# Optimization experiments

Hardware: AMD Instinct MI355X
Metric: run time of the kernel (lower is better)

Reference implementation:

```python
import jax, jax.numpy as jnp
import numpy as np

B, P, Q, O, H = 2048, 32, 65, 16, 32

def setup_inputs() -> dict:
    key = jax.random.key(0)
    ks = jax.random.split(key, 13)
    s1 = 1.0           # fan_in = 1 for Linear(1,H)
    sH = 1.0 / np.sqrt(H)
    return {
        "x": jax.random.normal(ks[0], (B, P), dtype=jnp.float32),
        # psi_{p,q}: 1 -> H -> H -> 1 MLPs, stacked over (P, Q)
        "psi_w1": jax.random.normal(ks[1], (P, Q, H), dtype=jnp.float32) * s1,
        "psi_b1": jax.random.normal(ks[2], (P, Q, H), dtype=jnp.float32) * s1,
        "psi_w2": jax.random.normal(ks[3], (P, Q, H, H), dtype=jnp.float32) * sH,
        "psi_b2": jax.random.normal(ks[4], (P, Q, H), dtype=jnp.float32) * sH,
        "psi_w3": jax.random.normal(ks[5], (P, Q, H), dtype=jnp.float32) * sH,
        "psi_b3": jax.random.normal(ks[6], (P, Q), dtype=jnp.float32) * sH,
        # phi_{q,i}: 1 -> H -> H -> 1 MLPs, stacked over (Q, O)
        "phi_w1": jax.random.normal(ks[7], (Q, O, H), dtype=jnp.float32) * s1,
        "phi_b1": jax.random.normal(ks[8], (Q, O, H), dtype=jnp.float32) * s1,
        "phi_w2": jax.random.normal(ks[9], (Q, O, H, H), dtype=jnp.float32) * sH,
        "phi_b2": jax.random.normal(ks[10], (Q, O, H), dtype=jnp.float32) * sH,
        "phi_w3": jax.random.normal(ks[11], (Q, O, H), dtype=jnp.float32) * sH,
        "phi_b3": jax.random.normal(ks[12], (Q, O), dtype=jnp.float32) * sH,
    }

def reference(x, psi_w1, psi_b1, psi_w2, psi_b2, psi_w3, psi_b3,
              phi_w1, phi_b1, phi_w2, phi_b2, phi_w3, phi_b3):
    # Inner functions psi_{p,q}(x_p): all P*Q tiny MLPs batched together.
    h = jnp.tanh(x[:, :, None, None] * psi_w1 + psi_b1)                 # [B,P,Q,H]
    h = jnp.tanh(jnp.einsum('bpqh,pqhk->bpqk', h, psi_w2) + psi_b2)     # [B,P,Q,H]
    psi = jnp.einsum('bpqh,pqh->bpq', h, psi_w3) + psi_b3               # [B,P,Q]
    s = psi.sum(axis=1)                                                 # [B,Q]  (sum over p)
    # Outer functions phi_{q,i}(s_q): all Q*O tiny MLPs batched together.
    g = jnp.tanh(s[:, :, None, None] * phi_w1 + phi_b1)                 # [B,Q,O,H]
    g = jnp.tanh(jnp.einsum('bqoh,qohk->bqok', g, phi_w2) + phi_b2)     # [B,Q,O,H]
    phi = jnp.einsum('bqoh,qoh->bqo', g, phi_w3) + phi_b3               # [B,Q,O]
    return phi.sum(axis=1)                                              # [B,O]  (sum over q)
```

## Files before the change

kernel.cpp:

```cpp
#include <hip/hip_runtime.h>
#include <hip/hip_bf16.h>

#define B_ 2048
#define P_ 32
#define Q_ 65
#define O_ 16
#define H_ 32

typedef __attribute__((ext_vector_type(8))) short short8;
typedef __attribute__((ext_vector_type(4))) float f32x4;

union F4S8 { float4 f; short8 s; unsigned u[4]; };

#if defined(__has_builtin)
# if __has_builtin(__builtin_amdgcn_exp2f)
#  define HAVE_EXP2 1
# endif
#endif
#ifdef HAVE_EXP2
#define SCALE_K 2.8853900817779268f
__device__ __forceinline__ float exp_z(float y) { return __builtin_amdgcn_exp2f(y); }
#else
#define SCALE_K 2.0f
__device__ __forceinline__ float exp_z(float y) { return __expf(y); }
#endif

__device__ __forceinline__ float sigc(float y) {
    return __builtin_amdgcn_rcpf(exp_z(y) + 1.0f);
}

__device__ __forceinline__ unsigned short bf_rne(float f) {
    unsigned u = __float_as_uint(f);
    return (unsigned short)((u + 0x7FFFu + ((u >> 16) & 1u)) >> 16);
}

__device__ __forceinline__ unsigned pk_bf16(float a, float b) {
    __hip_bfloat162 h = __float22bfloat162_rn(make_float2(a, b));
    return *reinterpret_cast<unsigned*>(&h);
}

struct Rec {
    float4 w1a, w1b, b1a, b1b;
    float4 h0, l0, h1, l1;
    float4 ms;
};

template<int MODE>
__device__ __forceinline__ Rec load_rec(
    const float* __restrict__ fragc, const float* __restrict__ shw,
    const float* __restrict__ w1, const float* __restrict__ b1,
    const float* __restrict__ w2, const float* __restrict__ b2,
    const float* __restrict__ w3,
    int pq, int lane, int g, int col)
{
    Rec r;
    if (MODE == 2) {
        const float4* fp = reinterpret_cast<const float4*>(fragc) + (size_t)pq * 256 + lane;
        r.h0 = fp[0]; r.l0 = fp[64]; r.h1 = fp[128]; r.l1 = fp[192];
        const float4* a = reinterpret_cast<const float4*>(shw + (size_t)pq * 128);
        r.w1a = a[g * 2];     r.w1b = a[g * 2 + 1];
        r.b1a = a[8 + g * 2]; r.b1b = a[8 + g * 2 + 1];
        r.ms  = a[16 + col];
    } else {
        const float4* w1p = reinterpret_cast<const float4*>(w1 + pq * H_ + g * 8);
        r.w1a = w1p[0]; r.w1b = w1p[1];
        const float4* b1p = reinterpret_cast<const float4*>(b1 + pq * H_ + g * 8);
        r.b1a = b1p[0]; r.b1b = b1p[1];
        const float* w2p = w2 + (size_t)pq * (H_ * H_);
        F4S8 u0, u1, u2, u3;
        float cs0 = 0.f, cs1 = 0.f;
        #pragma unroll
        for (int jj = 0; jj < 8; ++jj) {
            float v0 = -2.f * SCALE_K * w2p[(g * 8 + jj) * H_ + col];
            float v1 = -2.f * SCALE_K * w2p[(g * 8 + jj) * H_ + 16 + col];
            unsigned q0 = __float_as_uint(v0);
            u0.s[jj] = (short)(q0 >> 16);
            u1.s[jj] = (short)(__float_as_uint(v0 - __uint_as_float(q0 & 0xFFFF0000u)) >> 16);
            unsigned q1 = __float_as_uint(v1);
            u2.s[jj] = (short)(q1 >> 16);
            u3.s[jj] = (short)(__float_as_uint(v1 - __uint_as_float(q1 & 0xFFFF0000u)) >> 16);
        }
        for (int h = 0; h < H_; ++h) {
            cs0 += w2p[h * H_ + col];
            cs1 += w2p[h * H_ + 16 + col];
        }
        r.h0 = u0.f; r.l0 = u1.f; r.h1 = u2.f; r.l1 = u3.f;
        r.ms = make_float4(SCALE_K * (b2[pq * H_ + col] + cs0),
                           SCALE_K * (b2[pq * H_ + 16 + col] + cs1),
                           -2.f * w3[pq * H_ + col],
                           -2.f * w3[pq * H_ + 16 + col]);
    }
    return r;
}

template<bool PRE>
__device__ __forceinline__ void eval_rec(const Rec& r, float xv, float psum[4])
{
    float s0 = sigc(PRE ? fmaf(xv, r.w1a.x, r.b1a.x) : SCALE_K * fmaf(xv, r.w1a.x, r.b1a.x));
    float s1 = sigc(PRE ? fmaf(xv, r.w1a.y, r.b1a.y) : SCALE_K * fmaf(xv, r.w1a.y, r.b1a.y));
    float s2 = sigc(PRE ? fmaf(xv, r.w1a.z, r.b1a.z) : SCALE_K * fmaf(xv, r.w1a.z, r.b1a.z));
    float s3 = sigc(PRE ? fmaf(xv, r.w1a.w, r.b1a.w) : SCALE_K * fmaf(xv, r.w1a.w, r.b1a.w));
    float s4 = sigc(PRE ? fmaf(xv, r.w1b.x, r.b1b.x) : SCALE_K * fmaf(xv, r.w1b.x, r.b1b.x));
    float s5 = sigc(PRE ? fmaf(xv, r.w1b.y, r.b1b.y) : SCALE_K * fmaf(xv, r.w1b.y, r.b1b.y));
    float s6 = sigc(PRE ? fmaf(xv, r.w1b.z, r.b1b.z) : SCALE_K * fmaf(xv, r.w1b.z, r.b1b.z));
    float s7 = sigc(PRE ? fmaf(xv, r.w1b.w, r.b1b.w) : SCALE_K * fmaf(xv, r.w1b.w, r.b1b.w));

    F4S8 hi, lo;
    hi.u[0] = pk_bf16(s0, s1); hi.u[1] = pk_bf16(s2, s3);
    hi.u[2] = pk_bf16(s4, s5); hi.u[3] = pk_bf16(s6, s7);
    float l0v = s0 - __uint_as_float(hi.u[0] << 16);
    float l1v = s1 - __uint_as_float(hi.u[0] & 0xFFFF0000u);
    float l2v = s2 - __uint_as_float(hi.u[1] << 16);
    float l3v = s3 - __uint_as_float(hi.u[1] & 0xFFFF0000u);
    float l4v = s4 - __uint_as_float(hi.u[2] << 16);
    float l5v = s5 - __uint_as_float(hi.u[2] & 0xFFFF0000u);
    float l6v = s6 - __uint_as_float(hi.u[3] << 16);
    float l7v = s7 - __uint_as_float(hi.u[3] & 0xFFFF0000u);
    lo.u[0] = pk_bf16(l0v, l1v); lo.u[1] = pk_bf16(l2v, l3v);
    lo.u[2] = pk_bf16(l4v, l5v); lo.u[3] = pk_bf16(l6v, l7v);

    F4S8 c0, c1, c2, c3;
    c0.f = r.h0; c1.f = r.l0; c2.f = r.h1; c3.f = r.l1;
    f32x4 acc0 = {r.ms.x, r.ms.x, r.ms.x, r.ms.x};
    f32x4 acc1 = {r.ms.y, r.ms.y, r.ms.y, r.ms.y};
    acc0 = __builtin_amdgcn_mfma_f32_16x16x32_bf16(hi.s, c0.s, acc0, 0, 0, 0);
    acc0 = __builtin_amdgcn_mfma_f32_16x16x32_bf16(lo.s, c0.s, acc0, 0, 0, 0);
    acc0 = __builtin_amdgcn_mfma_f32_16x16x32_bf16(hi.s, c1.s, acc0, 0, 0, 0);
    acc1 = __builtin_amdgcn_mfma_f32_16x16x32_bf16(hi.s, c2.s, acc1, 0, 0, 0);
    acc1 = __builtin_amdgcn_mfma_f32_16x16x32_bf16(lo.s, c2.s, acc1, 0, 0, 0);
    acc1 = __builtin_amdgcn_mfma_f32_16x16x32_bf16(hi.s, c3.s, acc1, 0, 0, 0);

    #pragma unroll
    for (int rr = 0; rr < 4; ++rr) {
        psum[rr] = fmaf(sigc(acc0[rr]), r.ms.z, psum[rr]);
        psum[rr] = fmaf(sigc(acc1[rr]), r.ms.w, psum[rr]);
    }
}

__device__ __forceinline__ void reduce_store(float psum[4], float b3sum,
                                             int lane, int g, int b0w,
                                             float* addr_base, int stride, bool atomic)
{
    #pragma unroll
    for (int rr = 0; rr < 4; ++rr) {
        psum[rr] += __shfl_xor(psum[rr], 1);
        psum[rr] += __shfl_xor(psum[rr], 2);
        psum[rr] += __shfl_xor(psum[rr], 4);
        psum[rr] += __shfl_xor(psum[rr], 8);
    }
    float v01 = (lane & 1) ? psum[1] : psum[0];
    float v23 = (lane & 1) ? psum[3] : psum[2];
    float v = (lane & 2) ? v23 : v01;
    if ((lane & 15) < 4) {
        int row = b0w + g * 4 + (lane & 3);
        float* a = addr_base + (size_t)row * stride;
        if (atomic) atomicAdd(a, v + b3sum);
        else        *a = v + b3sum;
    }
}

template<int MODE>
__global__ __launch_bounds__(256)
void psi_main(const float* __restrict__ x, const float* __restrict__ xT,
              const float* __restrict__ w1, const float* __restrict__ b1,
              const float* __restrict__ w2, const float* __restrict__ b2,
              const float* __restrict__ w3, const float* __restrict__ b3,
              const float* __restrict__ b3c,
              const float* __restrict__ fragc, const float* __restrict__ shw,
              float* __restrict__ sT)
{
    const int id = blockIdx.x;
    const int j = (id & 7) * 260 + (id >> 3);
    const int q = j >> 5;
    const int btile = j & 31;
    const int lane = threadIdx.x & 63;
    const int wid = threadIdx.x >> 6;
    const int g = lane >> 4, col = lane & 15;
    const int b0w = btile * 64 + wid * 16;

    float psum[4] = {0.f, 0.f, 0.f, 0.f};
    float b3sum = (MODE == 2) ? b3c[q] : 0.f;

    Rec cur = load_rec<MODE>(fragc, shw, w1, b1, w2, b2, w3, q, lane, g, col);
    float xv = (MODE == 2) ? xT[b0w + col] : x[(size_t)(b0w + col) * P_];

    #pragma unroll 2
    for (int p = 0; p < P_; ++p) {
        const int pn = (p + 1 < P_) ? p + 1 : P_ - 1;
        Rec nxt = load_rec<MODE>(fragc, shw, w1, b1, w2, b2, w3,
                                 pn * Q_ + q, lane, g, col);
        float xn = (MODE == 2) ? xT[(size_t)pn * B_ + b0w + col]
                               : x[(size_t)(b0w + col) * P_ + pn];
        if (MODE != 2) {
            float ws = 0.f;
            for (int h = 0; h < H_; ++h) ws += w3[(p * Q_ + q) * H_ + h];
            b3sum += b3[p * Q_ + q] + ws;
        }
        eval_rec<(MODE == 2)>(cur, xv, psum);
        cur = nxt; xv = xn;
    }

    reduce_store(psum, b3sum, lane, g, b0w, sT + (size_t)q * B_, 1, false);
}

template<int MODE>
__global__ __launch_bounds__(256)
void phi_main(const float* __restrict__ sT,
              const float* __restrict__ w1, const float* __restrict__ b1,
              const float* __restrict__ w2, const float* __restrict__ b2,
              const float* __restrict__ w3, const float* __restrict__ b3,
              const float* __restrict__ b3g,
              const float* __restrict__ fragc, const float* __restrict__ shw,
              float* __restrict__ out)
{
    const int id = blockIdx.x;
    const int j = (id & 7) * 256 + (id >> 3);
    const int qg = j >> 9;
    const int rem = j & 511;
    const int o = rem >> 5;
    const int btile = rem & 31;
    const int lane = threadIdx.x & 63;
    const int wid = threadIdx.x >> 6;
    const int g = lane >> 4, col = lane & 15;
    const int b0w = btile * 64 + wid * 16;

    const int q0  = (qg == 0) ? 0 : 17 + (qg - 1) * 16;
    const int len = (qg == 0) ? 17 : 16;

    float psum[4] = {0.f, 0.f, 0.f, 0.f};
    float b3sum = (MODE == 2) ? b3g[qg * O_ + o] : 0.f;

    Rec cur = load_rec<MODE>(fragc, shw, w1, b1, w2, b2, w3, q0 * O_ + o, lane, g, col);
    float sv = sT[(size_t)q0 * B_ + b0w + col];

    #pragma unroll 2
    for (int i = 0; i < len; ++i) {
        const int in_ = (i + 1 < len) ? i + 1 : len - 1;
        const int qn = q0 + in_;
        Rec nxt = load_rec<MODE>(fragc, shw, w1, b1, w2, b2, w3,
                                 qn * O_ + o, lane, g, col);
        float sn = sT[(size_t)qn * B_ + b0w + col];
        if (MODE != 2) {
            float ws = 0.f;
            for (int h = 0; h < H_; ++h) ws += w3[((q0 + i) * O_ + o) * H_ + h];
            b3sum += b3[(q0 + i) * O_ + o] + ws;
        }
        eval_rec<(MODE == 2)>(cur, sv, psum);
        cur = nxt; sv = sn;
    }

    reduce_store(psum, b3sum, lane, g, b0w, out + o, O_, true);
}

__device__ __forceinline__ void do_frag(const float* __restrict__ w2,
                                        float* __restrict__ frag, int idx)
{
    int pq = idx >> 6, lane = idx & 63;
    int g = lane >> 4, col = lane & 15;
    const float* Wp = w2 + (size_t)pq * (H_ * H_);
    short8 h0v, l0v, h1v, l1v;
    #pragma unroll
    for (int jj = 0; jj < 8; ++jj) {
        float v0 = -2.f * SCALE_K * Wp[(g * 8 + jj) * H_ + col];
        float v1 = -2.f * SCALE_K * Wp[(g * 8 + jj) * H_ + 16 + col];
        unsigned short hb0 = bf_rne(v0);
        h0v[jj] = (short)hb0;
        l0v[jj] = (short)bf_rne(v0 - __uint_as_float(((unsigned)hb0) << 16));
        unsigned short hb1 = bf_rne(v1);
        h1v[jj] = (short)hb1;
        l1v[jj] = (short)bf_rne(v1 - __uint_as_float(((unsigned)hb1) << 16));
    }
    F4S8 a, b, c, d; a.s = h0v; b.s = l0v; c.s = h1v; d.s = l1v;
    float4* op = reinterpret_cast<float4*>(frag) + (size_t)pq * 256 + lane;
    op[0] = a.f; op[64] = b.f; op[128] = c.f; op[192] = d.f;
}

__device__ __forceinline__ void do_shw(const float* __restrict__ w1,
                                       const float* __restrict__ b1,
                                       const float* __restrict__ w2,
                                       const float* __restrict__ b2,
                                       const float* __restrict__ w3,
                                       float* __restrict__ shw, int idx)
{
    int pq = idx >> 7, i = idx & 127;
    float v;
    if (i < 32)       v = SCALE_K * w1[pq * H_ + i];
    else if (i < 64)  v = SCALE_K * b1[pq * H_ + (i - 32)];
    else {
        int c = (i - 64) >> 2, rr = i & 3;
        if (rr <= 1) {
            int cc = c + (rr == 1 ? 16 : 0);
            float cs = 0.f;
            const float* Wp = w2 + (size_t)pq * (H_ * H_);
            for (int h = 0; h < H_; ++h) cs += Wp[h * H_ + cc];
            v = SCALE_K * (b2[pq * H_ + cc] + cs);
        } else {
            int cc = c + (rr == 3 ? 16 : 0);
            v = -2.f * w3[pq * H_ + cc];
        }
    }
    shw[(size_t)pq * 128 + i] = v;
}

#define C1 133120
#define C2 199680
#define C3 465920
#define C4 599040
#define C5 664576
#define C6 664641
#define C7 664705

__global__ __launch_bounds__(256)
void prep_all(const float* __restrict__ psi_w1, const float* __restrict__ psi_b1,
              const float* __restrict__ psi_w2, const float* __restrict__ psi_b2,
              const float* __restrict__ psi_w3, const float* __restrict__ psi_b3,
              const float* __restrict__ phi_w1, const float* __restrict__ phi_b1,
              const float* __restrict__ phi_w2, const float* __restrict__ phi_b2,
              const float* __restrict__ phi_w3, const float* __restrict__ phi_b3,
              const float* __restrict__ x,
              float* __restrict__ fr1, float* __restrict__ fr2,
              float* __restrict__ sh1, float* __restrict__ sh2,
              float* __restrict__ xT, float* __restrict__ b3c,
              float* __restrict__ b3g)
{
    int t = blockIdx.x * 256 + threadIdx.x;
    if (t < C1) {
        do_frag(psi_w2, fr1, t);
    } else if (t < C2) {
        do_frag(phi_w2, fr2, t - C1);
    } else if (t < C3) {
        do_shw(psi_w1, psi_b1, psi_w2, psi_b2, psi_w3, sh1, t - C2);
    } else if (t < C4) {
        do_shw(phi_w1, phi_b1, phi_w2, phi_b2, phi_w3, sh2, t - C3);
    } else if (t < C5) {
        int idx = t - C4;
        int b = idx >> 5, p = idx & 31;
        xT[(size_t)p * B_ + b] = x[idx];
    } else if (t < C6) {
        int q = t - C5;
        float s = 0.f;
        for (int p = 0; p < P_; ++p) {
            int pq = p * Q_ + q;
            s += psi_b3[pq];
            for (int h = 0; h < H_; ++h) s += psi_w3[pq * H_ + h];
        }
        b3c[q] = s;
    } else if (t < C7) {
        int idx = t - C6;
        int qg = idx >> 4, o = idx & 15;
        int q0  = (qg == 0) ? 0 : 17 + (qg - 1) * 16;
        int len = (qg == 0) ? 17 : 16;
        float s = 0.f;
        for (int i = 0; i < len; ++i) {
            int qo = (q0 + i) * O_ + o;
            s += phi_b3[qo];
            for (int h = 0; h < H_; ++h) s += phi_w3[qo * H_ + h];
        }
        b3g[idx] = s;
    }
}

extern "C" void kernel_launch(void* const* d_in, const int* in_sizes, int n_in,
                              void* d_out, int out_size, void* d_ws, size_t ws_size,
                              hipStream_t stream) {
    const float* x      = (const float*)d_in[0];
    const float* psi_w1 = (const float*)d_in[1];
    const float* psi_b1 = (const float*)d_in[2];
    const float* psi_w2 = (const float*)d_in[3];
    const float* psi_b2 = (const float*)d_in[4];
    const float* psi_w3 = (const float*)d_in[5];
    const float* psi_b3 = (const float*)d_in[6];
    const float* phi_w1 = (const float*)d_in[7];
    const float* phi_b1 = (const float*)d_in[8];
    const float* phi_w2 = (const float*)d_in[9];
    const float* phi_b2 = (const float*)d_in[10];
    const float* phi_w3 = (const float*)d_in[11];
    const float* phi_b3 = (const float*)d_in[12];
    float* out = (float*)d_out;

    const size_t ST  = (size_t)B_ * Q_ * sizeof(float);
    const size_t XT  = (size_t)B_ * P_ * sizeof(float);
    const size_t FR1 = (size_t)P_ * Q_ * 64 * 64;
    const size_t FR2 = (size_t)Q_ * O_ * 64 * 64;
    const size_t SH1 = (size_t)P_ * Q_ * 128 * 4;
    const size_t SH2 = (size_t)Q_ * O_ * 128 * 4;
    const size_t B3C = 320;
    const size_t B3G = 320;

    float* sT = (float*)d_ws;
    hipMemsetAsync(out, 0, (size_t)B_ * O_ * sizeof(float), stream);

    if (ws_size >= ST + XT + FR1 + FR2 + SH1 + SH2 + B3C + B3G) {
        char* base = (char*)d_ws + ST;
        float* xTp  = (float*)base;                   base += XT;
        float* fr1  = (float*)base;                   base += FR1;
        float* fr2  = (float*)base;                   base += FR2;
        float* sh1  = (float*)base;                   base += SH1;
        float* sh2  = (float*)base;                   base += SH2;
        float* b3c  = (float*)base;                   base += B3C;
        float* b3g  = (float*)base;

        prep_all<<<(C7 + 255) / 256, 256, 0, stream>>>(
            psi_w1, psi_b1, psi_w2, psi_b2, psi_w3, psi_b3,
            phi_w1, phi_b1, phi_w2, phi_b2, phi_w3, phi_b3,
            x, fr1, fr2, sh1, sh2, xTp, b3c, b3g);

        psi_main<2><<<2080, 256, 0, stream>>>(
            x, xTp, psi_w1, psi_b1, psi_w2, psi_b2, psi_w3, psi_b3, b3c,
            fr1, sh1, sT);
        phi_main<2><<<2048, 256, 0, stream>>>(
            sT, phi_w1, phi_b1, phi_w2, phi_b2, phi_w3, phi_b3, b3g,
            fr2, sh2, out);
    } else {
        psi_main<0><<<2080, 256, 0, stream>>>(
            x, x, psi_w1, psi_b1, psi_w2, psi_b2, psi_w3, psi_b3, (const float*)sT,
            sT, sT, sT);
        phi_main<0><<<2048, 256, 0, stream>>>(
            sT, phi_w1, phi_b1, phi_w2, phi_b2, phi_w3, phi_b3, (const float*)sT,
            sT, sT, out);
    }
}
```

Baseline: 247.8 us.

## Halve block size for main kernels and parallelize prep column and bias sums

The psi and phi kernels now launch 128-thread blocks covering 32 batch rows each, with twice as many blocks and an occupancy hint of 8 blocks per CU, so the tail and scheduling are finer-grained. In the prep kernel, the W2 column sums are fused into the fragment-conversion threads using shuffles instead of a serial 32-iteration loop per thread. The b3 constant sums are split across a full wave with shuffle reductions rather than one thread looping serially. The risks are higher per-block overhead and more redundant weight loads per batch row in the main kernels.

After: 256.1 us. +3.4%, slower.

```diff
diff --git a/kernel.cpp b/kernel.cpp
--- a/kernel.cpp
+++ b/kernel.cpp
@@ -160,7 +160,7 @@
 }
 
 template<int MODE>
-__global__ __launch_bounds__(256)
+__global__ __launch_bounds__(128, 8)
 void psi_main(const float* __restrict__ x, const float* __restrict__ xT,
               const float* __restrict__ w1, const float* __restrict__ b1,
               const float* __restrict__ w2, const float* __restrict__ b2,
@@ -170,13 +170,13 @@
               float* __restrict__ sT)
 {
     const int id = blockIdx.x;
-    const int j = (id & 7) * 260 + (id >> 3);
-    const int q = j >> 5;
-    const int btile = j & 31;
+    const int j = (id & 7) * 520 + (id >> 3);
+    const int q = j >> 6;
+    const int btile = j & 63;
     const int lane = threadIdx.x & 63;
     const int wid = threadIdx.x >> 6;
     const int g = lane >> 4, col = lane & 15;
-    const int b0w = btile * 64 + wid * 16;
+    const int b0w = btile * 32 + wid * 16;
 
     float psum[4] = {0.f, 0.f, 0.f, 0.f};
     float b3sum = (MODE == 2) ? b3c[q] : 0.f;
@@ -204,7 +204,7 @@
 }
 
 template<int MODE>
-__global__ __launch_bounds__(256)
+__global__ __launch_bounds__(128, 8)
 void phi_main(const float* __restrict__ sT,
               const float* __restrict__ w1, const float* __restrict__ b1,
               const float* __restrict__ w2, const float* __restrict__ b2,
@@ -214,15 +214,15 @@
               float* __restrict__ out)
 {
     const int id = blockIdx.x;
-    const int j = (id & 7) * 256 + (id >> 3);
-    const int qg = j >> 9;
-    const int rem = j & 511;
-    const int o = rem >> 5;
-    const int btile = rem & 31;
+    const int j = (id & 7) * 512 + (id >> 3);
+    const int qg = j >> 10;
+    const int rem = j & 1023;
+    const int o = rem >> 6;
+    const int btile = rem & 63;
     const int lane = threadIdx.x & 63;
     const int wid = threadIdx.x >> 6;
     const int g = lane >> 4, col = lane & 15;
-    const int b0w = btile * 64 + wid * 16;
+    const int b0w = btile * 32 + wid * 16;
 
     const int q0  = (qg == 0) ? 0 : 17 + (qg - 1) * 16;
     const int len = (qg == 0) ? 17 : 16;
@@ -253,16 +253,22 @@
 }
 
 __device__ __forceinline__ void do_frag(const float* __restrict__ w2,
-                                        float* __restrict__ frag, int idx)
+                                        const float* __restrict__ b2,
+                                        float* __restrict__ frag,
+                                        float* __restrict__ shw, int idx)
 {
     int pq = idx >> 6, lane = idx & 63;
     int g = lane >> 4, col = lane & 15;
     const float* Wp = w2 + (size_t)pq * (H_ * H_);
     short8 h0v, l0v, h1v, l1v;
+    float cs0 = 0.f, cs1 = 0.f;
     #pragma unroll
     for (int jj = 0; jj < 8; ++jj) {
-        float v0 = -2.f * SCALE_K * Wp[(g * 8 + jj) * H_ + col];
-        float v1 = -2.f * SCALE_K * Wp[(g * 8 + jj) * H_ + 16 + col];
+        float w0 = Wp[(g * 8 + jj) * H_ + col];
+        float w1v = Wp[(g * 8 + jj) * H_ + 16 + col];
+        cs0 += w0; cs1 += w1v;
+        float v0 = -2.f * SCALE_K * w0;
+        float v1 = -2.f * SCALE_K * w1v;
         unsigned short hb0 = bf_rne(v0);
         h0v[jj] = (short)hb0;
         l0v[jj] = (short)bf_rne(v0 - __uint_as_float(((unsigned)hb0) << 16));
@@ -273,33 +279,30 @@
     F4S8 a, b, c, d; a.s = h0v; b.s = l0v; c.s = h1v; d.s = l1v;
     float4* op = reinterpret_cast<float4*>(frag) + (size_t)pq * 256 + lane;
     op[0] = a.f; op[64] = b.f; op[128] = c.f; op[192] = d.f;
+
+    cs0 += __shfl_xor(cs0, 16); cs0 += __shfl_xor(cs0, 32);
+    cs1 += __shfl_xor(cs1, 16); cs1 += __shfl_xor(cs1, 32);
+    if (g == 0) {
+        shw[(size_t)pq * 128 + 64 + col * 4 + 0] = SCALE_K * (b2[pq * H_ + col] + cs0);
+        shw[(size_t)pq * 128 + 64 + col * 4 + 1] = SCALE_K * (b2[pq * H_ + 16 + col] + cs1);
+    }
 }
 
 __device__ __forceinline__ void do_shw(const float* __restrict__ w1,
                                        const float* __restrict__ b1,
-                                       const float* __restrict__ w2,
-                                       const float* __restrict__ b2,
                                        const float* __restrict__ w3,
                                        float* __restrict__ shw, int idx)
 {
     int pq = idx >> 7, i = idx & 127;
-    float v;
-    if (i < 32)       v = SCALE_K * w1[pq * H_ + i];
-    else if (i < 64)  v = SCALE_K * b1[pq * H_ + (i - 32)];
+    if (i < 32)       shw[(size_t)pq * 128 + i] = SCALE_K * w1[pq * H_ + i];
+    else if (i < 64)  shw[(size_t)pq * 128 + i] = SCALE_K * b1[pq * H_ + (i - 32)];
     else {
         int c = (i - 64) >> 2, rr = i & 3;
-        if (rr <= 1) {
-            int cc = c + (rr == 1 ? 16 : 0);
-            float cs = 0.f;
-            const float* Wp = w2 + (size_t)pq * (H_ * H_);
-            for (int h = 0; h < H_; ++h) cs += Wp[h * H_ + cc];
-            v = SCALE_K * (b2[pq * H_ + cc] + cs);
-        } else {
+        if (rr >= 2) {
             int cc = c + (rr == 3 ? 16 : 0);
-            v = -2.f * w3[pq * H_ + cc];
-        }
-    }
-    shw[(size_t)pq * 128 + i] = v;
+            shw[(size_t)pq * 128 + i] = -2.f * w3[pq * H_ + cc];
+        }
+    }
 }
 
 #define C1 133120
@@ -307,8 +310,8 @@
 #define C3 465920
 #define C4 599040
 #define C5 664576
-#define C6 664641
-#define C7 664705
+#define C6 668736
+#define C7 672832
 
 __global__ __launch_bounds__(256)
 void prep_all(const float* __restrict__ psi_w1, const float* __restrict__ psi_b1,
@@ -325,38 +328,50 @@
 {
     int t = blockIdx.x * 256 + threadIdx.x;
     if (t < C1) {
-        do_frag(psi_w2, fr1, t);
+        do_frag(psi_w2, psi_b2, fr1, sh1, t);
     } else if (t < C2) {
-        do_frag(phi_w2, fr2, t - C1);
+        do_frag(phi_w2, phi_b2, fr2, sh2, t - C1);
     } else if (t < C3) {
-        do_shw(psi_w1, psi_b1, psi_w2, psi_b2, psi_w3, sh1, t - C2);
+        do_shw(psi_w1, psi_b1, psi_w3, sh1, t - C2);
     } else if (t < C4) {
-        do_shw(phi_w1, phi_b1, phi_w2, phi_b2, phi_w3, sh2, t - C3);
+        do_shw(phi_w1, phi_b1, phi_w3, sh2, t - C3);
     } else if (t < C5) {
         int idx = t - C4;
         int b = idx >> 5, p = idx & 31;
         xT[(size_t)p * B_ + b] = x[idx];
     } else if (t < C6) {
-        int q = t - C5;
-        float s = 0.f;
-        for (int p = 0; p < P_; ++p) {
-            int pq = p * Q_ + q;
-            s += psi_b3[pq];
-            for (int h = 0; h < H_; ++h) s += psi_w3[pq * H_ + h];
-        }
-        b3c[q] = s;
+        int idx = t - C5;
+        int q = idx >> 6, l = idx & 63;
+        int p = l >> 1, half = l & 1;
+        int pq = p * Q_ + q;
+        float s = half ? 0.f : psi_b3[pq];
+        const float* wp = psi_w3 + pq * H_ + half * 16;
+        #pragma unroll
+        for (int h = 0; h < 16; ++h) s += wp[h];
+        s += __shfl_xor(s, 1);  s += __shfl_xor(s, 2);  s += __shfl_xor(s, 4);
+        s += __shfl_xor(s, 8);  s += __shfl_xor(s, 16); s += __shfl_xor(s, 32);
+        if (l == 0) b3c[q] = s;
     } else if (t < C7) {
         int idx = t - C6;
-        int qg = idx >> 4, o = idx & 15;
+        int w = idx >> 6, l = idx & 63;
+        int qg = w >> 4, o = w & 15;
         int q0  = (qg == 0) ? 0 : 17 + (qg - 1) * 16;
-        int len = (qg == 0) ? 17 : 16;
-        float s = 0.f;
-        for (int i = 0; i < len; ++i) {
-            int qo = (q0 + i) * O_ + o;
-            s += phi_b3[qo];
-            for (int h = 0; h < H_; ++h) s += phi_w3[qo * H_ + h];
-        }
-        b3g[idx] = s;
+        int i = l >> 2, quarter = l & 3;
+        int qo = (q0 + i) * O_ + o;
+        float s = (quarter == 0) ? phi_b3[qo] : 0.f;
+        const float* wp = phi_w3 + qo * H_ + quarter * 8;
+        #pragma unroll
+        for (int h = 0; h < 8; ++h) s += wp[h];
+        if (qg == 0 && i == 15) {
+            int qo2 = (q0 + 16) * O_ + o;
+            if (quarter == 0) s += phi_b3[qo2];
+            const float* wp2 = phi_w3 + qo2 * H_ + quarter * 8;
+            #pragma unroll
+            for (int h = 0; h < 8; ++h) s += wp2[h];
+        }
+        s += __shfl_xor(s, 1);  s += __shfl_xor(s, 2);  s += __shfl_xor(s, 4);
+        s += __shfl_xor(s, 8);  s += __shfl_xor(s, 16); s += __shfl_xor(s, 32);
+        if (l == 0) b3g[qg * O_ + o] = s;
     }
 }
 
@@ -405,17 +420,17 @@
             phi_w1, phi_b1, phi_w2, phi_b2, phi_w3, phi_b3,
             x, fr1, fr2, sh1, sh2, xTp, b3c, b3g);
 
-        psi_main<2><<<2080, 256, 0, stream>>>(
+        psi_main<2><<<4160, 128, 0, stream>>>(
             x, xTp, psi_w1, psi_b1, psi_w2, psi_b2, psi_w3, psi_b3, b3c,
             fr1, sh1, sT);
-        phi_main<2><<<2048, 256, 0, stream>>>(
+        phi_main<2><<<4096, 128, 0, stream>>>(
             sT, phi_w1, phi_b1, phi_w2, phi_b2, phi_w3, phi_b3, b3g,
             fr2, sh2, out);
     } else {
-        psi_main<0><<<2080, 256, 0, stream>>>(
+        psi_main<0><<<4160, 128, 0, stream>>>(
             x, x, psi_w1, psi_b1, psi_w2, psi_b2, psi_w3, psi_b3, (const float*)sT,
             sT, sT, sT);
-        phi_main<0><<<2048, 256, 0, stream>>>(
+        phi_main<0><<<4096, 128, 0, stream>>>(
             sT, phi_w1, phi_b1, phi_w2, phi_b2, phi_w3, phi_b3, (const float*)sT,
             sT, sT, out);
     }
```
